# Kernel tuning notes

Hardware: AMD Instinct MI355X
Metric: run time of the kernel (lower is better)

Reference implementation:

```python
import jax, jax.numpy as jnp
import numpy as np

BN_EPS = 1e-5
W_SCALE = 0.05  # keep pre-softmax logits in a sane range with random weights


def setup_inputs() -> dict:
    key = jax.random.key(0)
    ks = jax.random.split(key, 8)
    b, C, H, W = 2, 512, 80, 80
    Ck, Cv, Co = 256, 256, 512
    return {
        "x": jax.random.normal(ks[0], (b, C, H, W), dtype=jnp.float32),
        "wk": jax.random.normal(ks[1], (Ck, C), dtype=jnp.float32) * W_SCALE,
        "bk": jax.random.normal(ks[2], (Ck,), dtype=jnp.float32) * W_SCALE,
        "gamma": jnp.ones((Ck,), dtype=jnp.float32),
        "beta": jnp.zeros((Ck,), dtype=jnp.float32),
        "rmean": jnp.zeros((Ck,), dtype=jnp.float32),
        "rvar": jnp.ones((Ck,), dtype=jnp.float32),
        "wv": jax.random.normal(ks[3], (Cv, C), dtype=jnp.float32) * W_SCALE,
        "bv": jax.random.normal(ks[4], (Cv,), dtype=jnp.float32) * W_SCALE,
        "wW": jax.random.normal(ks[5], (Co, Cv), dtype=jnp.float32) * W_SCALE,
        "bW": jax.random.normal(ks[6], (Co,), dtype=jnp.float32) * W_SCALE,
    }


def reference(x, wk, bk, gamma, beta, rmean, rvar, wv, bv, wW, bW):
    b, C, H, Wd = x.shape
    N = H * Wd
    Ck = wk.shape[0]
    Cv = wv.shape[0]
    # f_key == f_query (shared module): 1x1 conv + BN(inference) + ReLU
    k = jnp.einsum('bchw,oc->bohw', x, wk) + bk[:, None, None]
    scale_bn = gamma / jnp.sqrt(rvar + BN_EPS)
    k = (k - rmean[:, None, None]) * scale_bn[:, None, None] + beta[:, None, None]
    k = jax.nn.relu(k).reshape(b, Ck, N)          # [b, Ck, N]
    q = jnp.transpose(k, (0, 2, 1))               # [b, N, Ck] (query shares weights with key)
    # f_value: plain 1x1 conv
    v = (jnp.einsum('bchw,oc->bohw', x, wv) + bv[:, None, None]).reshape(b, Cv, N)
    sim = jnp.einsum('bnc,bcm->bnm', q, k) * (Ck ** -0.5)  # [b, N, N]
    sim = jax.nn.softmax(sim, axis=-1)
    ctx = jnp.einsum('bnm,bvm->bvn', sim, v).reshape(b, Cv, H, Wd)
    out = jnp.einsum('bvhw,ov->bohw', ctx, wW) + bW[:, None, None]
    return out
```

## Files before the change

kernel.cpp:

```cpp
#include <hip/hip_runtime.h>
#include <stdint.h>

typedef __attribute__((ext_vector_type(8))) short bf16x8;
typedef __attribute__((ext_vector_type(4))) float f32x4;

__device__ __forceinline__ ushort f2bf(float f) {
    union { float f; uint32_t i; } v; v.f = f;
    uint32_t r = v.i + 0x7fff + ((v.i >> 16) & 1);
    return (ushort)(r >> 16);
}
__device__ __forceinline__ uint32_t cvtpk(float lo, float hi) {
    uint32_t r;
    asm("v_cvt_pk_bf16_f32 %0, %1, %2" : "=v"(r) : "v"(lo), "v"(hi));
    return r;
}

typedef unsigned int uint_as1 __attribute__((address_space(1)));
typedef unsigned int uint_as3 __attribute__((address_space(3)));
__device__ __forceinline__ void async16(const void* g, void* l) {
    __builtin_amdgcn_global_load_lds((const uint_as1*)g, (uint_as3*)l, 16, 0, 0);
}

__global__ void prep_all(const float* __restrict__ wk, const float* __restrict__ wv,
                         const float* __restrict__ wW,
                         const float* __restrict__ bk, const float* __restrict__ gamma,
                         const float* __restrict__ beta, const float* __restrict__ rmean,
                         const float* __restrict__ rvar,
                         ushort* __restrict__ wkb, ushort* __restrict__ wvb,
                         ushort* __restrict__ wWb,
                         float* __restrict__ scaleA, float* __restrict__ shiftA) {
    const int b = blockIdx.x;
    if (b == 1536) {
        int i = threadIdx.x;
        float s = gamma[i] * rsqrtf(rvar[i] + 1e-5f);
        scaleA[i] = 0.25f * s;
        shiftA[i] = 0.25f * ((bk[i] - rmean[i]) * s + beta[i]);
        return;
    }
    const int i = (b & 511) * 256 + threadIdx.x;
    const float* src = (b < 512) ? wk : (b < 1024) ? wv : wW;
    ushort* dst = (b < 512) ? wkb : (b < 1024) ? wvb : wWb;
    dst[i] = f2bf(src[i]);
}

__global__ void transpose_cvt(const float* __restrict__ x, ushort* __restrict__ xt) {
    __shared__ float t[32][33];
    int b = blockIdx.z;
    int n0 = blockIdx.x * 32, c0 = blockIdx.y * 32;
    const float* xb = x + (size_t)b * 512 * 6400;
    ushort* xtb = xt + (size_t)b * 6400 * 512;
    int tx = threadIdx.x, ty = threadIdx.y;
    t[ty][tx] = xb[(size_t)(c0 + ty) * 6400 + n0 + tx];
    __syncthreads();
    xtb[(size_t)(n0 + ty) * 512 + c0 + tx] = f2bf(t[tx][ty]);
}

template <int EPI>
__global__ __launch_bounds__(256) void gemm_nt(
    const ushort* __restrict__ A, const ushort* __restrict__ B, void* __restrict__ Cout,
    int K, int lda, int ldb, int ldc,
    size_t zsa, size_t zsb, size_t zsc,
    const float* __restrict__ vec0, const float* __restrict__ vec1,
    float* __restrict__ rsum) {
    if (EPI == 6 && blockIdx.x < blockIdx.y) return;

    __shared__ __align__(16) ushort smem[6 * 4096];

    A += (size_t)blockIdx.z * zsa;
    B += (size_t)blockIdx.z * zsb;

    const int tid = threadIdx.x;
    const int lane = tid & 63, wave = tid >> 6;
    const int wm = wave & 1, wn = wave >> 1;
    const int bM = blockIdx.y * 128, bN = blockIdx.x * 128;

    const int sr = lane >> 2;
    const int scs = ((lane & 3) ^ ((lane >> 3) & 3)) * 8;
    const ushort* gA0 = A + (size_t)(bM + wave * 32 + sr) * lda + scs;
    const ushort* gA1 = gA0 + (size_t)16 * lda;
    const ushort* gB0 = B + (size_t)(bN + wave * 32 + sr) * ldb + scs;
    const ushort* gB1 = gB0 + (size_t)16 * ldb;
    ushort* lAw = &smem[wave * 1024];
    ushort* lBw = &smem[3 * 4096 + wave * 1024];

    const int rowA = wm * 64;
    const int rowB = wn * 64;
    const int fr = lane & 15;
    const int fk = ((lane >> 4) ^ ((fr >> 1) & 3)) * 8;

    f32x4 acc[4][4] = {};
    const int nT = K >> 5;

    auto stage = [&](int t, int buf) {
        const int k0 = t * 32;
        const int ob = buf * 4096;
        async16(gA0 + k0, lAw + ob);
        async16(gA1 + k0, lAw + ob + 512);
        async16(gB0 + k0, lBw + ob);
        async16(gB1 + k0, lBw + ob + 512);
    };

    stage(0, 0);
    if (nT > 1) stage(1, 1);

    for (int t = 0; t < nT; ++t) {
        if (t + 1 < nT) { asm volatile("s_waitcnt vmcnt(4)" ::: "memory"); }
        else            { asm volatile("s_waitcnt vmcnt(0)" ::: "memory"); }
        __builtin_amdgcn_sched_barrier(0);
        __builtin_amdgcn_s_barrier();
        __builtin_amdgcn_sched_barrier(0);
        if (t + 2 < nT) stage(t + 2, (t + 2) % 3);
        const int cur = t % 3;
        const ushort* lA = &smem[cur * 4096];
        const ushort* lB = &smem[3 * 4096 + cur * 4096];
        bf16x8 af[4], bff[4];
#pragma unroll
        for (int mi = 0; mi < 4; mi++)
            af[mi] = *(const bf16x8*)&lA[(rowA + mi * 16 + fr) * 32 + fk];
#pragma unroll
        for (int ni = 0; ni < 4; ni++)
            bff[ni] = *(const bf16x8*)&lB[(rowB + ni * 16 + fr) * 32 + fk];
#pragma unroll
        for (int mi = 0; mi < 4; mi++)
#pragma unroll
            for (int ni = 0; ni < 4; ni++)
                acc[mi][ni] = __builtin_amdgcn_mfma_f32_16x16x32_bf16(af[mi], bff[ni], acc[mi][ni], 0, 0, 0);
        __builtin_amdgcn_sched_barrier(0);
    }
    __builtin_amdgcn_s_barrier();
    __builtin_amdgcn_sched_barrier(0);

    float* Cf = (float*)Cout + (size_t)blockIdx.z * zsc;
    ushort* Cu = (ushort*)Cout + (size_t)blockIdx.z * zsc;
    float* lt = (float*)smem;
    const int g4 = (lane >> 4) * 4;
    const int cl = lane & 15;
    const int lr = tid >> 3;
    const int ch = tid & 7;

    if (EPI == 6) {
        const bool diag = (blockIdx.x == blockIdx.y);
        float creg[16];
#pragma unroll
        for (int i = 0; i < 16; i++) creg[i] = 0.f;
#pragma unroll
        for (int mi = 0; mi < 4; ++mi) {
#pragma unroll
            for (int ni = 0; ni < 4; ++ni) {
                const int lcol = wn * 64 + ni * 16 + cl;
#pragma unroll
                for (int r = 0; r < 4; ++r)
                    lt[(wm * 16 + g4 + r) * 132 + lcol] = acc[mi][ni][r];
            }
            __syncthreads();
            const int brow = (lr < 16) ? (mi * 16 + lr) : (64 + mi * 16 + (lr - 16));
            const int grow = bM + brow;
            const int gcol = bN + ch * 16;
            float vv[16];
#pragma unroll
            for (int i = 0; i < 16; i += 4) {
                f32x4 q = *(const f32x4*)&lt[lr * 132 + ch * 16 + i];
                vv[i] = __expf(q[0]); vv[i + 1] = __expf(q[1]);
                vv[i + 2] = __expf(q[2]); vv[i + 3] = __expf(q[3]);
            }
            float ssum = 0.f;
#pragma unroll
            for (int i = 0; i < 16; i++) { ssum += vv[i]; creg[i] += vv[i]; }
            ssum += __shfl_down(ssum, 4, 8);
            ssum += __shfl_down(ssum, 2, 8);
            ssum += __shfl_down(ssum, 1, 8);
            if (ch == 0) rsum[(size_t)blockIdx.x * 6400 + grow] = ssum;
            uint4 q0 = { cvtpk(vv[0], vv[1]), cvtpk(vv[2], vv[3]),
                         cvtpk(vv[4], vv[5]), cvtpk(vv[6], vv[7]) };
            uint4 q1 = { cvtpk(vv[8], vv[9]), cvtpk(vv[10], vv[11]),
                         cvtpk(vv[12], vv[13]), cvtpk(vv[14], vv[15]) };
            *(uint4*)&Cu[(size_t)grow * ldc + gcol] = q0;
            *(uint4*)&Cu[(size_t)grow * ldc + gcol + 8] = q1;
            if (!diag) {
#pragma unroll
                for (int i = 0; i < 16; i++) lt[lr * 132 + ch * 16 + i] = vv[i];
                __syncthreads();
                const int j = tid >> 1, h = tid & 1;
                ushort mo[16];
#pragma unroll
                for (int i = 0; i < 16; i += 2) {
                    float a = lt[(h * 16 + i) * 132 + j];
                    float b2 = lt[(h * 16 + i + 1) * 132 + j];
                    *(uint32_t*)&mo[i] = cvtpk(a, b2);
                }
                const size_t mbase = (size_t)(bN + j) * ldc + bM + h * 64 + mi * 16;
                *(uint4*)&Cu[mbase] = *(const uint4*)&mo[0];
                *(uint4*)&Cu[mbase + 8] = *(const uint4*)&mo[8];
            }
            __syncthreads();
        }
        if (!diag) {
#pragma unroll
            for (int i = 0; i < 16; i++) lt[lr * 132 + ch * 16 + i] = creg[i];
            __syncthreads();
            if (tid < 128) {
                float s = 0.f;
#pragma unroll
                for (int r = 0; r < 32; r++) s += lt[r * 132 + tid];
                rsum[(size_t)blockIdx.y * 6400 + bN + tid] = s;
            }
        }
        return;
    }

#pragma unroll
    for (int mi = 0; mi < 4; ++mi) {
#pragma unroll
        for (int ni = 0; ni < 4; ++ni) {
            const int lcol = wn * 64 + ni * 16 + cl;
#pragma unroll
            for (int r = 0; r < 4; ++r)
                lt[(wm * 16 + g4 + r) * 132 + lcol] = acc[mi][ni][r];
        }
        __syncthreads();
        {
            const int brow = (lr < 16) ? (mi * 16 + lr) : (64 + mi * 16 + (lr - 16));
            const int grow = bM + brow;
            const int gcol = bN + ch * 16;
            float vv[16];
#pragma unroll
            for (int i = 0; i < 16; i += 4) {
                f32x4 q = *(const f32x4*)&lt[lr * 132 + ch * 16 + i];
                vv[i] = q[0]; vv[i + 1] = q[1]; vv[i + 2] = q[2]; vv[i + 3] = q[3];
            }
            if (EPI == 1) {
#pragma unroll
                for (int i = 0; i < 16; i++)
                    vv[i] = fmaxf(vv[i] * vec0[gcol + i] + vec1[gcol + i], 0.f);
            }
            if (EPI == 2 || EPI == 3) {
                const float rb = vec0[grow];
#pragma unroll
                for (int i = 0; i < 16; i++) vv[i] += rb;
            }
            if (EPI == 3 || EPI == 4) {
#pragma unroll
                for (int i = 0; i < 16; i += 4) {
                    f32x4 q = { vv[i], vv[i + 1], vv[i + 2], vv[i + 3] };
                    *(f32x4*)&Cf[(size_t)grow * ldc + gcol + i] = q;
                }
            } else {
                uint4 q0 = { cvtpk(vv[0], vv[1]), cvtpk(vv[2], vv[3]),
                             cvtpk(vv[4], vv[5]), cvtpk(vv[6], vv[7]) };
                uint4 q1 = { cvtpk(vv[8], vv[9]), cvtpk(vv[10], vv[11]),
                             cvtpk(vv[12], vv[13]), cvtpk(vv[14], vv[15]) };
                *(uint4*)&Cu[(size_t)grow * ldc + gcol] = q0;
                *(uint4*)&Cu[(size_t)grow * ldc + gcol + 8] = q1;
            }
        }
        __syncthreads();
    }
}

__global__ __launch_bounds__(256) void reduce_ctx(const float* __restrict__ part, ushort* __restrict__ ctx,
                                                  const float* __restrict__ rsum) {
    const size_t CH = 1638400;
    size_t i = ((size_t)blockIdx.x * 256 + threadIdx.x) * 4;
    float4 a = *(const float4*)&part[i];
#pragma unroll
    for (int c = 1; c < 5; c++) {
        float4 s = *(const float4*)&part[i + (size_t)c * CH];
        a.x += s.x; a.y += s.y; a.z += s.z; a.w += s.w;
    }
    const int row = (int)(i >> 8);
    float s = 0.f;
#pragma unroll
    for (int xb = 0; xb < 50; xb++) s += rsum[(size_t)xb * 6400 + row];
    const float w = 1.f / s;
    uint2 o = { cvtpk(a.x * w, a.y * w), cvtpk(a.z * w, a.w * w) };
    *(uint2*)&ctx[i] = o;
}

extern "C" void kernel_launch(void* const* d_in, const int* in_sizes, int n_in,
                              void* d_out, int out_size, void* d_ws, size_t ws_size,
                              hipStream_t stream) {
    (void)in_sizes; (void)n_in; (void)out_size; (void)ws_size;
    const float* x     = (const float*)d_in[0];
    const float* wk    = (const float*)d_in[1];
    const float* bk    = (const float*)d_in[2];
    const float* gamma = (const float*)d_in[3];
    const float* beta  = (const float*)d_in[4];
    const float* rmean = (const float*)d_in[5];
    const float* rvar  = (const float*)d_in[6];
    const float* wv    = (const float*)d_in[7];
    const float* bv    = (const float*)d_in[8];
    const float* wW    = (const float*)d_in[9];
    const float* bW    = (const float*)d_in[10];
    float* out = (float*)d_out;

    ushort* Xt   = (ushort*)d_ws;
    ushort* wkb  = Xt + 6553600;
    ushort* wvb  = wkb + 131072;
    ushort* wWb  = wvb + 131072;
    ushort* Kt   = wWb + 131072;
    ushort* V    = Kt + 3276800;
    ushort* ctxT = V + 3276800;
    ushort* S    = ctxT + 3276800;
    float* scaleA = (float*)(S + 40960000);
    float* shiftA = scaleA + 256;
    float* rowsum = shiftA + 256;
    float* part   = rowsum + 320000;

    prep_all<<<1537, 256, 0, stream>>>(wk, wv, wW, bk, gamma, beta, rmean, rvar,
                                       wkb, wvb, wWb, scaleA, shiftA);
    transpose_cvt<<<dim3(200, 16, 2), dim3(32, 32), 0, stream>>>(x, Xt);

    gemm_nt<1><<<dim3(2, 50, 2), 256, 0, stream>>>(Xt, wkb, Kt, 512, 512, 512, 256,
                                                   3276800, 0, 1638400, scaleA, shiftA, nullptr);
    gemm_nt<2><<<dim3(50, 2, 2), 256, 0, stream>>>(wvb, Xt, V, 512, 512, 512, 6400,
                                                   0, 3276800, 1638400, bv, nullptr, nullptr);

    for (int b = 0; b < 2; b++) {
        ushort* Ktb  = Kt + (size_t)b * 1638400;
        ushort* Vb   = V  + (size_t)b * 1638400;
        ushort* ctxb = ctxT + (size_t)b * 1638400;
        gemm_nt<6><<<dim3(50, 50), 256, 0, stream>>>(Ktb, Ktb, S, 256, 256, 256, 6400,
                                                     0, 0, 0, nullptr, nullptr, rowsum);
        gemm_nt<4><<<dim3(2, 50, 5), 256, 0, stream>>>(S, Vb, part, 1280, 6400, 6400, 256,
                                                       1280, 1280, 1638400, nullptr, nullptr, nullptr);
        reduce_ctx<<<1600, 256, 0, stream>>>(part, ctxb, rowsum);
    }

    gemm_nt<3><<<dim3(50, 4, 2), 256, 0, stream>>>(wWb, ctxT, out, 256, 256, 256, 6400,
                                                   0, 1638400, 3276800, bW, nullptr, nullptr);
}
```

Baseline: 305.6 us.

## Merge K/V projection launches and overlap batch-1 sim GEMM with batch-0 PV

Refactors the GEMM into a device body that takes explicit block indices, so several GEMMs can run from one launch. The K and V projection GEMMs are merged into one 400-block kernel. The batch-1 similarity/exp GEMM now runs in the same launch as the batch-0 P·V GEMM, using separate S and rowsum buffers per batch. This is meant to fill the GPU better with small grids and cut launch gaps between stages. The cost is a second 80MB S buffer and more memory traffic and cache pressure while the two stages run together.

```diff
diff --git a/kernel.cpp b/kernel.cpp
--- a/kernel.cpp
+++ b/kernel.cpp
@@ -56,23 +56,21 @@
 }
 
 template <int EPI>
-__global__ __launch_bounds__(256) void gemm_nt(
+__device__ __forceinline__ void gemm_body(
+    int bxi, int byi, int bzi,
     const ushort* __restrict__ A, const ushort* __restrict__ B, void* __restrict__ Cout,
     int K, int lda, int ldb, int ldc,
     size_t zsa, size_t zsb, size_t zsc,
     const float* __restrict__ vec0, const float* __restrict__ vec1,
-    float* __restrict__ rsum) {
-    if (EPI == 6 && blockIdx.x < blockIdx.y) return;
-
-    __shared__ __align__(16) ushort smem[6 * 4096];
-
-    A += (size_t)blockIdx.z * zsa;
-    B += (size_t)blockIdx.z * zsb;
+    float* __restrict__ rsum, ushort* smem) {
+
+    A += (size_t)bzi * zsa;
+    B += (size_t)bzi * zsb;
 
     const int tid = threadIdx.x;
     const int lane = tid & 63, wave = tid >> 6;
     const int wm = wave & 1, wn = wave >> 1;
-    const int bM = blockIdx.y * 128, bN = blockIdx.x * 128;
+    const int bM = byi * 128, bN = bxi * 128;
 
     const int sr = lane >> 2;
     const int scs = ((lane & 3) ^ ((lane >> 3) & 3)) * 8;
@@ -130,8 +128,8 @@
     __builtin_amdgcn_s_barrier();
     __builtin_amdgcn_sched_barrier(0);
 
-    float* Cf = (float*)Cout + (size_t)blockIdx.z * zsc;
-    ushort* Cu = (ushort*)Cout + (size_t)blockIdx.z * zsc;
+    float* Cf = (float*)Cout + (size_t)bzi * zsc;
+    ushort* Cu = (ushort*)Cout + (size_t)bzi * zsc;
     float* lt = (float*)smem;
     const int g4 = (lane >> 4) * 4;
     const int cl = lane & 15;
@@ -139,7 +137,7 @@
     const int ch = tid & 7;
 
     if (EPI == 6) {
-        const bool diag = (blockIdx.x == blockIdx.y);
+        const bool diag = (bxi == byi);
         float creg[16];
 #pragma unroll
         for (int i = 0; i < 16; i++) creg[i] = 0.f;
@@ -169,7 +167,7 @@
             ssum += __shfl_down(ssum, 4, 8);
             ssum += __shfl_down(ssum, 2, 8);
             ssum += __shfl_down(ssum, 1, 8);
-            if (ch == 0) rsum[(size_t)blockIdx.x * 6400 + grow] = ssum;
+            if (ch == 0) rsum[(size_t)bxi * 6400 + grow] = ssum;
             uint4 q0 = { cvtpk(vv[0], vv[1]), cvtpk(vv[2], vv[3]),
                          cvtpk(vv[4], vv[5]), cvtpk(vv[6], vv[7]) };
             uint4 q1 = { cvtpk(vv[8], vv[9]), cvtpk(vv[10], vv[11]),
@@ -202,7 +200,7 @@
                 float s = 0.f;
 #pragma unroll
                 for (int r = 0; r < 32; r++) s += lt[r * 132 + tid];
-                rsum[(size_t)blockIdx.y * 6400 + bN + tid] = s;
+                rsum[(size_t)byi * 6400 + bN + tid] = s;
             }
         }
         return;
@@ -254,6 +252,53 @@
             }
         }
         __syncthreads();
+    }
+}
+
+template <int EPI>
+__global__ __launch_bounds__(256) void gemm_nt(
+    const ushort* __restrict__ A, const ushort* __restrict__ B, void* __restrict__ Cout,
+    int K, int lda, int ldb, int ldc,
+    size_t zsa, size_t zsb, size_t zsc,
+    const float* __restrict__ vec0, const float* __restrict__ vec1,
+    float* __restrict__ rsum) {
+    __shared__ __align__(16) ushort smem[6 * 4096];
+    if (EPI == 6 && blockIdx.x < blockIdx.y) return;
+    gemm_body<EPI>(blockIdx.x, blockIdx.y, blockIdx.z, A, B, Cout, K, lda, ldb, ldc,
+                   zsa, zsb, zsc, vec0, vec1, rsum, smem);
+}
+
+__global__ __launch_bounds__(256) void k_kv(
+    const ushort* __restrict__ Xt, const ushort* __restrict__ wkb,
+    const ushort* __restrict__ wvb, ushort* __restrict__ Kt, ushort* __restrict__ V,
+    const float* __restrict__ scaleA, const float* __restrict__ shiftA,
+    const float* __restrict__ bv) {
+    __shared__ __align__(16) ushort smem[6 * 4096];
+    const int id = blockIdx.x;
+    if (id < 200) {
+        gemm_body<1>(id & 1, (id >> 1) % 50, id / 100, Xt, wkb, Kt,
+                     512, 512, 512, 256, 3276800, 0, 1638400, scaleA, shiftA, nullptr, smem);
+    } else {
+        const int i = id - 200;
+        gemm_body<2>(i % 50, (i / 50) % 2, i / 100, wvb, Xt, V,
+                     512, 512, 512, 6400, 0, 3276800, 1638400, bv, nullptr, nullptr, smem);
+    }
+}
+
+__global__ __launch_bounds__(256) void k_pv_s(
+    const ushort* __restrict__ S0, const ushort* __restrict__ V0, float* __restrict__ part,
+    const ushort* __restrict__ Kt1, ushort* __restrict__ S1, float* __restrict__ rowsum1) {
+    __shared__ __align__(16) ushort smem[6 * 4096];
+    const int id = blockIdx.x;
+    if (id < 500) {
+        gemm_body<4>(id & 1, (id >> 1) % 50, id / 100, S0, V0, part,
+                     1280, 6400, 6400, 256, 1280, 1280, 1638400, nullptr, nullptr, nullptr, smem);
+    } else {
+        const int sid = id - 500;
+        const int sx = sid % 50, sy = sid / 50;
+        if (sx < sy) return;
+        gemm_body<6>(sx, sy, 0, Kt1, Kt1, S1,
+                     256, 256, 256, 6400, 0, 0, 0, nullptr, nullptr, rowsum1, smem);
     }
 }
 
@@ -300,31 +345,36 @@
     ushort* Kt   = wWb + 131072;
     ushort* V    = Kt + 3276800;
     ushort* ctxT = V + 3276800;
-    ushort* S    = ctxT + 3276800;
-    float* scaleA = (float*)(S + 40960000);
+    ushort* S0   = ctxT + 3276800;
+    ushort* S1   = S0 + 40960000;
+    float* scaleA = (float*)(S1 + 40960000);
     float* shiftA = scaleA + 256;
-    float* rowsum = shiftA + 256;
-    float* part   = rowsum + 320000;
+    float* rowsum0 = shiftA + 256;
+    float* rowsum1 = rowsum0 + 320000;
+    float* part   = rowsum1 + 320000;
 
     prep_all<<<1537, 256, 0, stream>>>(wk, wv, wW, bk, gamma, beta, rmean, rvar,
                                        wkb, wvb, wWb, scaleA, shiftA);
     transpose_cvt<<<dim3(200, 16, 2), dim3(32, 32), 0, stream>>>(x, Xt);
 
-    gemm_nt<1><<<dim3(2, 50, 2), 256, 0, stream>>>(Xt, wkb, Kt, 512, 512, 512, 256,
-                                                   3276800, 0, 1638400, scaleA, shiftA, nullptr);
-    gemm_nt<2><<<dim3(50, 2, 2), 256, 0, stream>>>(wvb, Xt, V, 512, 512, 512, 6400,
-                                                   0, 3276800, 1638400, bv, nullptr, nullptr);
-
-    for (int b = 0; b < 2; b++) {
-        ushort* Ktb  = Kt + (size_t)b * 1638400;
-        ushort* Vb   = V  + (size_t)b * 1638400;
-        ushort* ctxb = ctxT + (size_t)b * 1638400;
-        gemm_nt<6><<<dim3(50, 50), 256, 0, stream>>>(Ktb, Ktb, S, 256, 256, 256, 6400,
-                                                     0, 0, 0, nullptr, nullptr, rowsum);
-        gemm_nt<4><<<dim3(2, 50, 5), 256, 0, stream>>>(S, Vb, part, 1280, 6400, 6400, 256,
-                                                       1280, 1280, 1638400, nullptr, nullptr, nullptr);
-        reduce_ctx<<<1600, 256, 0, stream>>>(part, ctxb, rowsum);
-    }
+    k_kv<<<400, 256, 0, stream>>>(Xt, wkb, wvb, Kt, V, scaleA, shiftA, bv);
+
+    ushort* Kt0 = Kt;
+    ushort* Kt1 = Kt + 1638400;
+    ushort* V0b = V;
+    ushort* V1b = V + 1638400;
+
+    gemm_nt<6><<<dim3(50, 50), 256, 0, stream>>>(Kt0, Kt0, S0, 256, 256, 256, 6400,
+                                                 0, 0, 0, nullptr, nullptr, rowsum0);
+
+    k_pv_s<<<3000, 256, 0, stream>>>(S0, V0b, part, Kt1, S1, rowsum1);
+
+    reduce_ctx<<<1600, 256, 0, stream>>>(part, ctxT, rowsum0);
+
+    gemm_nt<4><<<dim3(2, 50, 5), 256, 0, stream>>>(S1, V1b, part, 1280, 6400, 6400, 256,
+                                                   1280, 1280, 1638400, nullptr, nullptr, nullptr);
+
+    reduce_ctx<<<1600, 256, 0, stream>>>(part, ctxT + 1638400, rowsum1);
 
     gemm_nt<3><<<dim3(50, 4, 2), 256, 0, stream>>>(wWb, ctxT, out, 256, 256, 256, 6400,
                                                    0, 1638400, 3276800, bW, nullptr, nullptr);
```

Measured after the change: 297.4 us. 2.7% less time.
